# Kernel optimization log

Measured on AMD Instinct MI355X. Metric: run time of the kernel, lower is better.

Reference implementation:

```python
import jax, jax.numpy as jnp
import numpy as np

B, S, C, H = 8, 1024, 512, 8
DH = C // H  # channels per head


def setup_inputs() -> dict:
    key = jax.random.key(0)
    ks = jax.random.split(key, 10)
    s = 1.0 / np.sqrt(C)
    return {
        "pe_lin_encoding": jax.random.normal(ks[0], (B, S, C), jnp.float32),
        "pe_lin_skip": jax.random.normal(ks[1], (B, S, C), jnp.float32),
        "Wq": jax.random.normal(ks[2], (C, C), jnp.float32) * s,
        "bq": jax.random.normal(ks[3], (C,), jnp.float32) * s,
        "Wk": jax.random.normal(ks[4], (C, C), jnp.float32) * s,
        "bk": jax.random.normal(ks[5], (C,), jnp.float32) * s,
        "Wv": jax.random.normal(ks[6], (C, C), jnp.float32) * s,
        "bv": jax.random.normal(ks[7], (C,), jnp.float32) * s,
        "Wo": jax.random.normal(ks[8], (C, C), jnp.float32) * s,
        "bo": jax.random.normal(ks[9], (C,), jnp.float32) * s,
    }


def reference(pe_lin_encoding, pe_lin_skip, Wq, bq, Wk, bk, Wv, bv, Wo, bo):
    # flatten trailing dims (already [B, S, C] here)
    x = pe_lin_encoding.reshape(pe_lin_encoding.shape[0], pe_lin_encoding.shape[1], -1)
    # torch Linear convention: y = x @ W^T + b, W is [out, in]
    q = jnp.einsum("bsc,oc->bso", x, Wq) + bq
    k = jnp.einsum("bsc,oc->bso", x, Wk) + bk
    v = jnp.einsum("bsc,oc->bso", x, Wv) + bv
    # split heads: [B, S, H, DH] -> attention per head
    q = q.reshape(B, S, H, DH)
    k = k.reshape(B, S, H, DH)
    v = v.reshape(B, S, H, DH)
    scale = 1.0 / np.sqrt(DH)
    scores = jnp.einsum("bqhd,bkhd->bhqk", q, k) * scale  # [B,H,S,S]
    attn = jax.nn.softmax(scores, axis=-1)
    ctx = jnp.einsum("bhqk,bkhd->bqhd", attn, v).reshape(B, S, C)
    out = jnp.einsum("bsc,oc->bso", ctx, Wo) + bo
    return out + pe_lin_skip
```

## Files before the change

kernel.cpp:

```cpp
#include <hip/hip_runtime.h>
#include <hip/hip_bf16.h>

typedef unsigned short u16;
typedef unsigned int u32;

constexpr int B  = 8;
constexpr int S  = 1024;
constexpr int C  = 512;
constexpr int H  = 8;
constexpr int DH = 64;
constexpr int M  = B * S;

typedef __attribute__((ext_vector_type(8))) short bf16x8;
typedef __attribute__((ext_vector_type(4))) float f32x4;
typedef __attribute__((ext_vector_type(16))) float f32x16;
typedef __attribute__((ext_vector_type(4))) u32 u32x4;

#define GLOBAL_AS __attribute__((address_space(1)))
#define LDS_AS    __attribute__((address_space(3)))

#define QSCALE 0.1803368867f

__device__ __forceinline__ float bf2f(u16 u) {
    return __uint_as_float(((u32)u) << 16);
}
__device__ __forceinline__ u16 f2bf(float f) {
    u32 u = __float_as_uint(f);
    u += 0x7fffu + ((u >> 16) & 1u);
    return (u16)(u >> 16);
}
__device__ __forceinline__ u32 pack2(float a, float b) {
    return (u32)f2bf(a) | ((u32)f2bf(b) << 16);
}
__device__ __forceinline__ u32 cvtpk(float a, float b) {
    u32 d;
    asm("v_cvt_pk_bf16_f32 %0, %1, %2" : "=v"(d) : "v"(a), "v"(b));
    return d;
}
__device__ __forceinline__ float fexp2(float x) {
#if __has_builtin(__builtin_amdgcn_exp2f)
    return __builtin_amdgcn_exp2f(x);
#else
    float r; asm("v_exp_f32 %0, %1" : "=v"(r) : "v"(x)); return r;
#endif
}
__device__ __forceinline__ void async_cp16(const u16* g, u16* l) {
    __builtin_amdgcn_global_load_lds((const GLOBAL_AS void*)g, (LDS_AS void*)l, 16, 0, 0);
}
__device__ __forceinline__ f32x16 zero16() {
    f32x16 z;
    #pragma unroll
    for (int i = 0; i < 16; i++) z[i] = 0.f;
    return z;
}

constexpr int NX4 = M * C / 4;
constexpr int NW4 = C * C / 4;

__global__ __launch_bounds__(256) void cvt_kernel(
    const float* __restrict__ x,
    const float* __restrict__ wq, const float* __restrict__ wk,
    const float* __restrict__ wv, const float* __restrict__ wo,
    u16* __restrict__ xb, u16* __restrict__ wqkv, u16* __restrict__ wob)
{
    const int i = blockIdx.x * 256 + threadIdx.x;
    const float* src; u16* dst; int off;
    if      (i < NX4)          { src = x;  dst = xb;           off = i; }
    else if (i < NX4 +   NW4)  { src = wq; dst = wqkv;         off = i - NX4; }
    else if (i < NX4 + 2*NW4)  { src = wk; dst = wqkv + C*C;   off = i - NX4 -   NW4; }
    else if (i < NX4 + 3*NW4)  { src = wv; dst = wqkv + 2*C*C; off = i - NX4 - 2*NW4; }
    else                       { src = wo; dst = wob;          off = i - NX4 - 3*NW4; }
    float4 v = ((const float4*)src)[off];
    uint2 p; p.x = pack2(v.x, v.y); p.y = pack2(v.z, v.w);
    ((uint2*)dst)[off] = p;
}

__global__ __launch_bounds__(256) void qkv_gemm(
    const u16* __restrict__ xb, const u16* __restrict__ wqkv,
    const float* __restrict__ bq, const float* __restrict__ bk,
    const float* __restrict__ bv,
    u16* __restrict__ Qo, u16* __restrict__ Ko, u16* __restrict__ Vo)
{
    __shared__ alignas(16) u16 smem[128 * 96];
    u16* const Asm = smem;
    u16* const Bsm = smem + 128 * 64;

    const int mTile = blockIdx.x * 128;
    const int nTile = blockIdx.y * 64;
    const int t = threadIdx.x, lane = t & 63, w = t >> 6;
    const int ql = lane & 15, quad = lane >> 4;
    const int wm = (w & 1) * 64, wn = (w >> 1) * 32;

    f32x4 acc[4][2];
    #pragma unroll
    for (int i = 0; i < 4; i++)
        #pragma unroll
        for (int j = 0; j < 2; j++) acc[i][j] = (f32x4){0.f, 0.f, 0.f, 0.f};

    for (int k0 = 0; k0 < C; k0 += 64) {
        __syncthreads();
        #pragma unroll
        for (int q = 0; q < 4; q++) {
            const int chunk = q * 256 + t;
            const int row = chunk >> 3, c8 = (chunk & 7) * 8;
            async_cp16(xb + (size_t)(mTile + row) * C + k0 + c8, &Asm[row * 64 + c8]);
        }
        #pragma unroll
        for (int q = 0; q < 2; q++) {
            const int chunk = q * 256 + t;
            const int row = chunk >> 3, c8 = (chunk & 7) * 8;
            async_cp16(wqkv + (size_t)(nTile + row) * C + k0 + c8, &Bsm[row * 64 + c8]);
        }
        __syncthreads();

        #pragma unroll
        for (int ks = 0; ks < 64; ks += 32) {
            bf16x8 af[4], bfr[2];
            #pragma unroll
            for (int i = 0; i < 4; i++)
                af[i] = *(const bf16x8*)&Asm[(wm + i*16 + ql) * 64 + ks + quad*8];
            #pragma unroll
            for (int j = 0; j < 2; j++)
                bfr[j] = *(const bf16x8*)&Bsm[(wn + j*16 + ql) * 64 + ks + quad*8];
            #pragma unroll
            for (int i = 0; i < 4; i++)
                #pragma unroll
                for (int j = 0; j < 2; j++)
                    acc[i][j] = __builtin_amdgcn_mfma_f32_16x16x32_bf16(af[i], bfr[j], acc[i][j], 0, 0, 0);
        }
    }

    const int z = nTile >> 9;
    const int nBase = nTile & 511;
    const int bb = mTile >> 10, ssBase = mTile & 1023;
    if (z == 2) {
        __syncthreads();
        u16* const T = smem;
        #pragma unroll
        for (int j = 0; j < 2; j++) {
            const int n = wn + j*16 + ql;
            const float bj = bv[nBase + n];
            #pragma unroll
            for (int i = 0; i < 4; i++)
                #pragma unroll
                for (int r = 0; r < 4; r++)
                    T[n * 136 + wm + i*16 + quad*4 + r] = f2bf(acc[i][j][r] + bj);
        }
        __syncthreads();
        #pragma unroll
        for (int q = 0; q < 4; q++) {
            const int c = q * 256 + t;
            const int row = c >> 4, col = (c & 15) * 8;
            const int o = nBase + row, h = o >> 6, d = o & 63;
            *(float4*)(Vo + ((size_t)((bb*H + h) * DH + d)) * S + ssBase + col) =
                *(const float4*)&T[row * 136 + col];
        }
    } else {
        const float* bias = (z == 0) ? bq : bk;
        u16* dst          = (z == 0) ? Qo : Ko;
        const float sc    = (z == 0) ? QSCALE : 1.0f;
        const int h = nBase >> 6;
        __syncthreads();
        u16* const T = smem;
        #pragma unroll
        for (int j = 0; j < 2; j++) {
            const int n = wn + j*16 + ql;
            const float bj = bias[nBase + n];
            #pragma unroll
            for (int i = 0; i < 4; i++)
                #pragma unroll
                for (int r = 0; r < 4; r++)
                    T[(wm + i*16 + quad*4 + r) * 72 + n] = f2bf((acc[i][j][r] + bj) * sc);
        }
        __syncthreads();
        #pragma unroll
        for (int q = 0; q < 4; q++) {
            const int c = q * 256 + t;
            const int row = c >> 3, col = (c & 7) * 8;
            *(float4*)(dst + ((size_t)((bb*H + h) * S + (ssBase + row))) * DH + col) =
                *(const float4*)&T[row * 72 + col];
        }
    }
}

__global__ __launch_bounds__(256) void attn_kernel(
    const u16* __restrict__ Qo,
    const u16* __restrict__ Ko,
    const u16* __restrict__ Vo,
    u16* __restrict__ ctx)
{
    __shared__ alignas(16) u16 KVs[2][2][2][64 * 64];

    const int g = blockIdx.x;
    const int xcd = g & 7, slot = g >> 3;
    const int bh = xcd * 8 + (slot >> 4);
    const int qt = slot & 15;

    const int t = threadIdx.x;
    const int lane = t & 63, w = t >> 6;
    const int qg = w & 1, kg = w >> 1;
    const int l31 = lane & 31, hi = lane >> 5;
    const int sxh8 = ((l31 & 7) ^ hi) << 3;
    const int kRow = l31 * 64;

    const u16* __restrict__ Qb = Qo + (size_t)bh * S * DH;
    const u16* __restrict__ Kb = Ko + (size_t)bh * S * DH;
    const u16* __restrict__ Vt = Vo + (size_t)bh * DH * S;

    const int qrow = qt * 64 + qg * 32 + l31;
    bf16x8 qf[4];
    #pragma unroll
    for (int ks = 0; ks < 4; ks++)
        qf[ks] = *(const bf16x8*)(Qb + (size_t)qrow * DH + ks * 16 + hi * 8);

    bf16x8 onesf;
    #pragma unroll
    for (int i = 0; i < 8; i++) onesf[i] = (short)0x3F80;

    f32x16 acc[2], accl;
    acc[0] = zero16(); acc[1] = zero16(); accl = zero16();

    const int tp = t & 127;
    const int kBase = kg * 512;

    auto STAGE = [&](int buf, int it) {
        const int k0 = kBase + it * 64;
        u16* const Kd = &KVs[buf][kg][0][0];
        u16* const Vd = &KVs[buf][kg][1][0];
        #pragma unroll
        for (int q = 0; q < 4; ++q) {
            const int gi = q * 128 + tp;
            const int row = gi >> 3, cc = gi & 7;
            const int c = cc ^ (row & 7);
            async_cp16(Kb + (size_t)(k0 + row) * DH + c * 8, &Kd[gi * 8]);
            async_cp16(Vt + (size_t)row * S + k0 + c * 8,    &Vd[gi * 8]);
        }
    };

    STAGE(0, 0);
    #pragma unroll 2
    for (int it = 0; it < 8; ++it) {
        const int cur = it & 1;
        if (it + 1 < 8) {
            STAGE(cur ^ 1, it + 1);
            asm volatile("s_waitcnt vmcnt(8)" ::: "memory");
        } else {
            asm volatile("s_waitcnt vmcnt(0)" ::: "memory");
        }
        asm volatile("s_barrier" ::: "memory");

        const u16* const Kh = &KVs[cur][kg][0][0];
        const u16* const Vh = &KVs[cur][kg][1][0];

        #pragma unroll
        for (int kt = 0; kt < 2; ++kt) {
            f32x16 sc = zero16();
            #pragma unroll
            for (int ks = 0; ks < 4; ++ks) {
                const bf16x8 kf = *(const bf16x8*)&Kh[kRow + kt * 2048 + ((ks << 4) ^ sxh8)];
                sc = __builtin_amdgcn_mfma_f32_32x32x16_bf16(kf, qf[ks], sc, 0, 0, 0);
            }
            #pragma unroll
            for (int s = 0; s < 2; ++s) {
                float e0 = fexp2(sc[8*s+0]), e1 = fexp2(sc[8*s+1]);
                float e2 = fexp2(sc[8*s+2]), e3 = fexp2(sc[8*s+3]);
                float e4 = fexp2(sc[8*s+4]), e5 = fexp2(sc[8*s+5]);
                float e6 = fexp2(sc[8*s+6]), e7 = fexp2(sc[8*s+7]);
                u32 x0 = cvtpk(e0, e1), x1 = cvtpk(e2, e3);
                u32 y0 = cvtpk(e4, e5), y1 = cvtpk(e6, e7);
                asm("v_permlane32_swap_b32 %0, %1" : "+v"(x0), "+v"(y0));
                asm("v_permlane32_swap_b32 %0, %1" : "+v"(x1), "+v"(y1));
                u32x4 pw; pw.x = x0; pw.y = x1; pw.z = y0; pw.w = y1;
                const bf16x8 pa = __builtin_bit_cast(bf16x8, pw);

                const int ccol = (((kt * 4 + s * 2) << 3) ^ sxh8);
                acc[0] = __builtin_amdgcn_mfma_f32_32x32x16_bf16(
                    pa, *(const bf16x8*)&Vh[kRow + ccol], acc[0], 0, 0, 0);
                acc[1] = __builtin_amdgcn_mfma_f32_32x32x16_bf16(
                    pa, *(const bf16x8*)&Vh[kRow + 2048 + ccol], acc[1], 0, 0, 0);
                accl = __builtin_amdgcn_mfma_f32_32x32x16_bf16(pa, onesf, accl, 0, 0, 0);
            }
        }
        asm volatile("s_barrier" ::: "memory");
    }

    __syncthreads();
    float* F = (float*)&KVs[0][0][0][0];
    if (kg == 1) {
        #pragma unroll
        for (int r = 0; r < 16; ++r) F[r * 128 + qg * 64 + lane] = acc[0][r];
        #pragma unroll
        for (int r = 0; r < 16; ++r) F[(16 + r) * 128 + qg * 64 + lane] = acc[1][r];
        #pragma unroll
        for (int r = 0; r < 16; ++r) F[(32 + r) * 128 + qg * 64 + lane] = accl[r];
    }
    __syncthreads();
    if (kg == 0) {
        #pragma unroll
        for (int r = 0; r < 16; ++r) acc[0][r] += F[r * 128 + qg * 64 + lane];
        #pragma unroll
        for (int r = 0; r < 16; ++r) acc[1][r] += F[(16 + r) * 128 + qg * 64 + lane];
        #pragma unroll
        for (int r = 0; r < 16; ++r) accl[r]   += F[(32 + r) * 128 + qg * 64 + lane];

        const int b_ = bh >> 3, h = bh & 7;
        const int qbase2 = qt * 64 + qg * 32 + 4 * hi;
        #pragma unroll
        for (int r = 0; r < 16; ++r) {
            const float inv = 1.0f / accl[r];
            const int srow = qbase2 + (r & 3) + 8 * (r >> 2);
            const size_t base = ((size_t)(b_ * S + srow)) * C + h * DH + l31;
            ctx[base]      = f2bf(acc[0][r] * inv);
            ctx[base + 32] = f2bf(acc[1][r] * inv);
        }
    }
}

__global__ __launch_bounds__(256) void out_gemm(
    const u16* __restrict__ ctx, const u16* __restrict__ wob,
    const float* __restrict__ bo, const float* __restrict__ skip,
    float* __restrict__ out)
{
    __shared__ alignas(16) u16 smem[8704];
    u16* const Asm = smem;
    u16* const Bsm = smem + 64 * 64;

    const int mTile = blockIdx.x * 64;
    const int nTile = blockIdx.y * 64;
    const int t = threadIdx.x, lane = t & 63, w = t >> 6;
    const int ql = lane & 15, quad = lane >> 4;
    const int wm = (w & 1) * 32, wn = (w >> 1) * 32;

    const int erow = t >> 4, ecol = (t & 15) * 4;
    float4 sk[4];
    #pragma unroll
    for (int q8 = 0; q8 < 4; ++q8)
        sk[q8] = *(const float4*)&skip[(size_t)(mTile + q8*16 + erow) * C + nTile + ecol];
    const float4 b4 = *(const float4*)&bo[nTile + ecol];

    f32x4 acc[2][2];
    #pragma unroll
    for (int i = 0; i < 2; i++)
        #pragma unroll
        for (int j = 0; j < 2; j++) acc[i][j] = (f32x4){0.f, 0.f, 0.f, 0.f};

    for (int k0 = 0; k0 < C; k0 += 64) {
        __syncthreads();
        #pragma unroll
        for (int q = 0; q < 2; q++) {
            const int chunk = q * 256 + t;
            const int row = chunk >> 3, c8 = (chunk & 7) * 8;
            async_cp16(ctx + (size_t)(mTile + row) * C + k0 + c8, &Asm[row * 64 + c8]);
        }
        #pragma unroll
        for (int q = 0; q < 2; q++) {
            const int chunk = q * 256 + t;
            const int row = chunk >> 3, c8 = (chunk & 7) * 8;
            async_cp16(wob + (size_t)(nTile + row) * C + k0 + c8, &Bsm[row * 64 + c8]);
        }
        __syncthreads();

        #pragma unroll
        for (int ks = 0; ks < 64; ks += 32) {
            bf16x8 af[2], bfr[2];
            #pragma unroll
            for (int i = 0; i < 2; i++)
                af[i] = *(const bf16x8*)&Asm[(wm + i*16 + ql) * 64 + ks + quad*8];
            #pragma unroll
            for (int j = 0; j < 2; j++)
                bfr[j] = *(const bf16x8*)&Bsm[(wn + j*16 + ql) * 64 + ks + quad*8];
            #pragma unroll
            for (int i = 0; i < 2; i++)
                #pragma unroll
                for (int j = 0; j < 2; j++)
                    acc[i][j] = __builtin_amdgcn_mfma_f32_16x16x32_bf16(af[i], bfr[j], acc[i][j], 0, 0, 0);
        }
    }

    float* const F2 = (float*)smem;
    __syncthreads();
    #pragma unroll
    for (int j = 0; j < 2; j++) {
        const int n = wn + j*16 + ql;
        #pragma unroll
        for (int i = 0; i < 2; i++)
            #pragma unroll
            for (int r = 0; r < 4; r++)
                F2[(wm + i*16 + quad*4 + r) * 68 + n] = acc[i][j][r];
    }
    __syncthreads();
    #pragma unroll
    for (int q8 = 0; q8 < 4; ++q8) {
        const int row = q8*16 + erow;
        const float4 v = *(const float4*)&F2[row * 68 + ecol];
        float4 r4;
        r4.x = v.x + b4.x + sk[q8].x;  r4.y = v.y + b4.y + sk[q8].y;
        r4.z = v.z + b4.z + sk[q8].z;  r4.w = v.w + b4.w + sk[q8].w;
        *(float4*)&out[(size_t)(mTile + row) * C + nTile + ecol] = r4;
    }
}

extern "C" void kernel_launch(void* const* d_in, const int* in_sizes, int n_in,
                              void* d_out, int out_size, void* d_ws, size_t ws_size,
                              hipStream_t stream) {
    (void)in_sizes; (void)n_in; (void)out_size; (void)ws_size;
    const float* x    = (const float*)d_in[0];
    const float* skip = (const float*)d_in[1];
    const float* Wq   = (const float*)d_in[2];
    const float* bq   = (const float*)d_in[3];
    const float* Wk   = (const float*)d_in[4];
    const float* bk   = (const float*)d_in[5];
    const float* Wv   = (const float*)d_in[6];
    const float* bv   = (const float*)d_in[7];
    const float* Wo   = (const float*)d_in[8];
    const float* bo   = (const float*)d_in[9];
    float* out = (float*)d_out;

    u16* xb   = (u16*)d_ws;
    u16* wqkv = xb   + (size_t)M * C;
    u16* wob  = wqkv + (size_t)3 * C * C;
    u16* Qo   = wob  + (size_t)C * C;
    u16* Ko   = Qo   + (size_t)B * H * S * DH;
    u16* Vo   = Ko   + (size_t)B * H * S * DH;
    u16* ctx  = xb;

    cvt_kernel<<<dim3((NX4 + 4 * NW4) / 256), 256, 0, stream>>>(
        x, Wq, Wk, Wv, Wo, xb, wqkv, wob);
    qkv_gemm<<<dim3(M / 128, 1536 / 64), 256, 0, stream>>>(
        xb, wqkv, bq, bk, bv, Qo, Ko, Vo);
    attn_kernel<<<dim3(1024), 256, 0, stream>>>(Qo, Ko, Vo, ctx);
    out_gemm<<<dim3(M / 64, C / 64), 256, 0, stream>>>(
        ctx, wob, bo, skip, out);
}
```

Baseline: 164.2 us.

## Compute Q, K and V for one head per block in the QKV GEMM

Each QKV GEMM block now covers a 64-row M tile and a single head, and computes the Q, K and V projections together over three 64-column weight slices. The shared A (activation) tile is loaded once and reused for all three projections, where before it was reloaded for each of the 24 N tiles. The grid becomes M/64 x 8 blocks with smaller M tiles and 24 accumulator fragments per thread. This changes the balance of A versus B reuse, register pressure and occupancy.

```diff
diff --git a/kernel.cpp b/kernel.cpp
--- a/kernel.cpp
+++ b/kernel.cpp
@@ -81,59 +81,91 @@
     const float* __restrict__ bv,
     u16* __restrict__ Qo, u16* __restrict__ Ko, u16* __restrict__ Vo)
 {
-    __shared__ alignas(16) u16 smem[128 * 96];
+    __shared__ alignas(16) u16 smem[64 * 64 + 3 * 64 * 64];
     u16* const Asm = smem;
-    u16* const Bsm = smem + 128 * 64;
-
-    const int mTile = blockIdx.x * 128;
-    const int nTile = blockIdx.y * 64;
+    u16* const Bsm = smem + 64 * 64;
+
+    const int mTile = blockIdx.x * 64;
+    const int h = blockIdx.y;
+    const int nBase = h * 64;
     const int t = threadIdx.x, lane = t & 63, w = t >> 6;
     const int ql = lane & 15, quad = lane >> 4;
-    const int wm = (w & 1) * 64, wn = (w >> 1) * 32;
-
-    f32x4 acc[4][2];
-    #pragma unroll
-    for (int i = 0; i < 4; i++)
-        #pragma unroll
-        for (int j = 0; j < 2; j++) acc[i][j] = (f32x4){0.f, 0.f, 0.f, 0.f};
+    const int wm = (w & 1) * 32, wn = (w >> 1) * 32;
+
+    f32x4 acc[3][2][2];
+    #pragma unroll
+    for (int z = 0; z < 3; z++)
+        #pragma unroll
+        for (int i = 0; i < 2; i++)
+            #pragma unroll
+            for (int j = 0; j < 2; j++) acc[z][i][j] = (f32x4){0.f, 0.f, 0.f, 0.f};
 
     for (int k0 = 0; k0 < C; k0 += 64) {
         __syncthreads();
         #pragma unroll
-        for (int q = 0; q < 4; q++) {
+        for (int q = 0; q < 2; q++) {
             const int chunk = q * 256 + t;
             const int row = chunk >> 3, c8 = (chunk & 7) * 8;
             async_cp16(xb + (size_t)(mTile + row) * C + k0 + c8, &Asm[row * 64 + c8]);
         }
         #pragma unroll
-        for (int q = 0; q < 2; q++) {
+        for (int q = 0; q < 6; q++) {
             const int chunk = q * 256 + t;
-            const int row = chunk >> 3, c8 = (chunk & 7) * 8;
-            async_cp16(wqkv + (size_t)(nTile + row) * C + k0 + c8, &Bsm[row * 64 + c8]);
+            const int z = chunk >> 9, rr = (chunk >> 3) & 63, c8 = (chunk & 7) * 8;
+            async_cp16(wqkv + (size_t)z * C * C + (size_t)(nBase + rr) * C + k0 + c8,
+                       &Bsm[z * 4096 + rr * 64 + c8]);
         }
         __syncthreads();
 
         #pragma unroll
         for (int ks = 0; ks < 64; ks += 32) {
-            bf16x8 af[4], bfr[2];
-            #pragma unroll
-            for (int i = 0; i < 4; i++)
+            bf16x8 af[2];
+            #pragma unroll
+            for (int i = 0; i < 2; i++)
                 af[i] = *(const bf16x8*)&Asm[(wm + i*16 + ql) * 64 + ks + quad*8];
             #pragma unroll
-            for (int j = 0; j < 2; j++)
-                bfr[j] = *(const bf16x8*)&Bsm[(wn + j*16 + ql) * 64 + ks + quad*8];
-            #pragma unroll
-            for (int i = 0; i < 4; i++)
+            for (int z = 0; z < 3; z++) {
+                bf16x8 bfr[2];
                 #pragma unroll
                 for (int j = 0; j < 2; j++)
-                    acc[i][j] = __builtin_amdgcn_mfma_f32_16x16x32_bf16(af[i], bfr[j], acc[i][j], 0, 0, 0);
-        }
-    }
-
-    const int z = nTile >> 9;
-    const int nBase = nTile & 511;
+                    bfr[j] = *(const bf16x8*)&Bsm[z * 4096 + (wn + j*16 + ql) * 64 + ks + quad*8];
+                #pragma unroll
+                for (int i = 0; i < 2; i++)
+                    #pragma unroll
+                    for (int j = 0; j < 2; j++)
+                        acc[z][i][j] = __builtin_amdgcn_mfma_f32_16x16x32_bf16(af[i], bfr[j], acc[z][i][j], 0, 0, 0);
+            }
+        }
+    }
+
     const int bb = mTile >> 10, ssBase = mTile & 1023;
-    if (z == 2) {
+    #pragma unroll
+    for (int z = 0; z < 2; ++z) {
+        const float* bias = z ? bk : bq;
+        u16* dst          = z ? Ko : Qo;
+        const float sc    = z ? 1.0f : QSCALE;
+        __syncthreads();
+        u16* const T = smem;
+        #pragma unroll
+        for (int j = 0; j < 2; j++) {
+            const int n = wn + j*16 + ql;
+            const float bj = bias[nBase + n];
+            #pragma unroll
+            for (int i = 0; i < 2; i++)
+                #pragma unroll
+                for (int r = 0; r < 4; r++)
+                    T[(wm + i*16 + quad*4 + r) * 72 + n] = f2bf((acc[z][i][j][r] + bj) * sc);
+        }
+        __syncthreads();
+        #pragma unroll
+        for (int q = 0; q < 2; q++) {
+            const int c = q * 256 + t;
+            const int row = c >> 3, col = (c & 7) * 8;
+            *(float4*)(dst + ((size_t)((bb*H + h) * S + (ssBase + row))) * DH + col) =
+                *(const float4*)&T[row * 72 + col];
+        }
+    }
+    {
         __syncthreads();
         u16* const T = smem;
         #pragma unroll
@@ -141,43 +173,17 @@
             const int n = wn + j*16 + ql;
             const float bj = bv[nBase + n];
             #pragma unroll
-            for (int i = 0; i < 4; i++)
+            for (int i = 0; i < 2; i++)
                 #pragma unroll
                 for (int r = 0; r < 4; r++)
-                    T[n * 136 + wm + i*16 + quad*4 + r] = f2bf(acc[i][j][r] + bj);
-        }
-        __syncthreads();
-        #pragma unroll
-        for (int q = 0; q < 4; q++) {
-            const int c = q * 256 + t;
-            const int row = c >> 4, col = (c & 15) * 8;
-            const int o = nBase + row, h = o >> 6, d = o & 63;
-            *(float4*)(Vo + ((size_t)((bb*H + h) * DH + d)) * S + ssBase + col) =
-                *(const float4*)&T[row * 136 + col];
-        }
-    } else {
-        const float* bias = (z == 0) ? bq : bk;
-        u16* dst          = (z == 0) ? Qo : Ko;
-        const float sc    = (z == 0) ? QSCALE : 1.0f;
-        const int h = nBase >> 6;
-        __syncthreads();
-        u16* const T = smem;
-        #pragma unroll
-        for (int j = 0; j < 2; j++) {
-            const int n = wn + j*16 + ql;
-            const float bj = bias[nBase + n];
-            #pragma unroll
-            for (int i = 0; i < 4; i++)
-                #pragma unroll
-                for (int r = 0; r < 4; r++)
-                    T[(wm + i*16 + quad*4 + r) * 72 + n] = f2bf((acc[i][j][r] + bj) * sc);
-        }
-        __syncthreads();
-        #pragma unroll
-        for (int q = 0; q < 4; q++) {
+                    T[n * 72 + wm + i*16 + quad*4 + r] = f2bf(acc[2][i][j][r] + bj);
+        }
+        __syncthreads();
+        #pragma unroll
+        for (int q = 0; q < 2; q++) {
             const int c = q * 256 + t;
             const int row = c >> 3, col = (c & 7) * 8;
-            *(float4*)(dst + ((size_t)((bb*H + h) * S + (ssBase + row))) * DH + col) =
+            *(float4*)(Vo + ((size_t)((bb*H + h) * DH + row)) * S + ssBase + col) =
                 *(const float4*)&T[row * 72 + col];
         }
     }
@@ -426,7 +432,7 @@
 
     cvt_kernel<<<dim3((NX4 + 4 * NW4) / 256), 256, 0, stream>>>(
         x, Wq, Wk, Wv, Wo, xb, wqkv, wob);
-    qkv_gemm<<<dim3(M / 128, 1536 / 64), 256, 0, stream>>>(
+    qkv_gemm<<<dim3(M / 64, H), 256, 0, stream>>>(
         xb, wqkv, bq, bk, bv, Qo, Ko, Vo);
     attn_kernel<<<dim3(1024), 256, 0, stream>>>(Qo, Ko, Vo, ctx);
     out_gemm<<<dim3(M / 64, C / 64), 256, 0, stream>>>(
```

Result: no change. 162.9 us (-0.8%).
